# Performance work log

Hardware: AMD Instinct MI355X
Metric: run time of the kernel (lower is better)

## Reference

```python
import jax, jax.numpy as jnp
import numpy as np

B, S, D, H = 128, 256, 256, 8   # graphs, nodes/graph, dim_h, heads
N = B * S
E = 524288
DH = D // H
BN_EPS = 1e-5

def _bn(v, g, b):
    # BatchNorm1d forward with batch statistics (biased var), eval-dropout model
    m = v.mean(0)
    var = v.var(0)
    return (v - m) * jax.lax.rsqrt(var + BN_EPS) * g + b

def setup_inputs() -> dict:
    key = jax.random.key(0)
    ks = jax.random.split(key, 40)
    x = jax.random.normal(ks[0], (N, D), jnp.float32)
    src = jax.random.randint(ks[1], (E,), 0, N)
    dst = (src // S) * S + jax.random.randint(ks[2], (E,), 0, S)  # intra-graph edges
    edge_index = jnp.stack([src, dst]).astype(jnp.int64)
    def lin(k, i, o):
        return (jax.random.normal(k, (i, o), jnp.float32) / np.float32(np.sqrt(i)))
    inp = {
        'x': x, 'edge_index': edge_index,
        'W_gcn': lin(ks[3], D, D), 'b_gcn': jnp.zeros((D,), jnp.float32),
        'W_gin1': lin(ks[4], D, D), 'b_gin1': jnp.zeros((D,), jnp.float32),
        'W_gin2': lin(ks[5], D, D), 'b_gin2': jnp.zeros((D,), jnp.float32),
        'g_kv': jnp.ones((D,), jnp.float32), 'be_kv': jnp.zeros((D,), jnp.float32),
        'Wq1': lin(ks[6], D, D), 'bq1': jnp.zeros((D,), jnp.float32),
        'Wq2': lin(ks[7], D, D), 'bq2': jnp.zeros((D,), jnp.float32),
        'Wq_a': lin(ks[8], D, D), 'bq_a': jnp.zeros((D,), jnp.float32),
        'Wk_a': lin(ks[9], D, D), 'bk_a': jnp.zeros((D,), jnp.float32),
        'Wv_a': lin(ks[10], D, D), 'bv_a': jnp.zeros((D,), jnp.float32),
        'Wo_a': lin(ks[11], D, D), 'bo_a': jnp.zeros((D,), jnp.float32),
        'g_attn': jnp.ones((D,), jnp.float32), 'be_attn': jnp.zeros((D,), jnp.float32),
        'Wf1': lin(ks[12], D, 2 * D), 'bf1': jnp.zeros((2 * D,), jnp.float32),
        'Wf2': lin(ks[13], 2 * D, D), 'bf2': jnp.zeros((D,), jnp.float32),
        'g2': jnp.ones((D,), jnp.float32), 'be2': jnp.zeros((D,), jnp.float32),
    }
    return inp

def _forward(x, edge_index,
             W_gcn, b_gcn, W_gin1, b_gin1, W_gin2, b_gin2, g_kv, be_kv,
             Wq1, bq1, Wq2, bq2,
             Wq_a, bq_a, Wk_a, bk_a, Wv_a, bv_a, Wo_a, bo_a, g_attn, be_attn,
             Wf1, bf1, Wf2, bf2, g2, be2):
    row, col = edge_index[0], edge_index[1]
    h_in1 = x

    # ---- expert 0: GCNConv (add self loops + symmetric norm) ----
    loops = jnp.arange(N, dtype=row.dtype)
    row2 = jnp.concatenate([row, loops])
    col2 = jnp.concatenate([col, loops])
    deg = jax.ops.segment_sum(jnp.ones_like(row2, jnp.float32), col2, num_segments=N)
    dinv = jnp.where(deg > 0, jax.lax.rsqrt(deg), 0.0)
    norm = dinv[row2] * dinv[col2]                     # [E+N]
    xw = x @ W_gcn                                      # [N, D]
    h_gcn = jax.ops.segment_sum(norm[:, None] * xw[row2], col2, num_segments=N) + b_gcn
    e0 = _bn(h_gcn, g_kv, be_kv)

    # ---- expert 1: GINConv (eps=0, sum aggregation, 2-layer MLP) ----
    agg = jax.ops.segment_sum(x[row], col, num_segments=N)
    h_gin = jax.nn.relu((x + agg) @ W_gin1 + b_gin1) @ W_gin2 + b_gin2
    e1 = _bn(h_gin, g_kv, be_kv)

    # ---- global expert normalization (torch .std -> unbiased) ----
    allo = jnp.concatenate([e0, e1], axis=0)
    gm = allo.mean()
    gs = jnp.std(allo, ddof=1)
    e0 = (e0 - gm) / (gs + 1e-8)
    e1 = (e1 - gm) / (gs + 1e-8)

    # ---- uniform routing & kv residual mix ----
    kv = 0.5 * e0 + 0.5 * e1 + 0.1 * h_in1              # [N, D]

    # ---- dense batching (equal-sized graphs -> pure reshape, full mask) ----
    q_dense = h_in1.reshape(B, S, D)
    kv_dense = kv.reshape(B, S, D)

    # ---- q projection MLP ----
    q_dense = jax.nn.relu(q_dense @ Wq1 + bq1) @ Wq2 + bq2

    # ---- multihead attention (batch_first, no padding) ----
    qh = (q_dense @ Wq_a + bq_a).reshape(B, S, H, DH)
    kh = (kv_dense @ Wk_a + bk_a).reshape(B, S, H, DH)
    vh = (kv_dense @ Wv_a + bv_a).reshape(B, S, H, DH)
    scores = jnp.einsum('bqhd,bkhd->bhqk', qh, kh) / np.float32(np.sqrt(DH))
    attn = jax.nn.softmax(scores, axis=-1)
    o = jnp.einsum('bhqk,bkhd->bqhd', attn, vh).reshape(B, S, D)
    h_attn = (o @ Wo_a + bo_a).reshape(N, D)

    # ---- residual + norm + FFN block ----
    h = _bn(h_in1 + h_attn, g_attn, be_attn)
    h_ff = jax.nn.relu(h @ Wf1 + bf1) @ Wf2 + bf2
    h = _bn(h + h_ff, g2, be2)
    return h

def reference(x, edge_index,
              W_gcn, b_gcn, W_gin1, b_gin1, W_gin2, b_gin2, g_kv, be_kv,
              Wq1, bq1, Wq2, bq2,
              Wq_a, bq_a, Wk_a, bk_a, Wv_a, bv_a, Wo_a, bo_a, g_attn, be_attn,
              Wf1, bf1, Wf2, bf2, g2, be2):
    return _forward(x, edge_index,
                    W_gcn, b_gcn, W_gin1, b_gin1, W_gin2, b_gin2, g_kv, be_kv,
                    Wq1, bq1, Wq2, bq2,
                    Wq_a, bq_a, Wk_a, bk_a, Wv_a, bv_a, Wo_a, bo_a, g_attn, be_attn,
                    Wf1, bf1, Wf2, bf2, g2, be2)
```

## Files before the change

### kernel.cpp

```cpp
#include <hip/hip_runtime.h>
#include <hip/hip_bf16.h>

typedef __hip_bfloat16 bf16;
typedef __attribute__((ext_vector_type(8))) short short8;
typedef __attribute__((ext_vector_type(4))) short short4v;
typedef __attribute__((ext_vector_type(4))) float f32x4;
typedef __attribute__((ext_vector_type(4))) int i32x4;

#define N_ 32768
#define D_ 256
#define S_ 256
#define B_ 128
#define E_ 524288

static __device__ __forceinline__ f32x4 mfma16(short8 a, short8 b, f32x4 c) {
  return __builtin_amdgcn_mfma_f32_16x16x32_bf16(a, b, c, 0, 0, 0);
}
static __device__ __forceinline__ f32x4 fzero4() {
  f32x4 z; z[0] = 0.f; z[1] = 0.f; z[2] = 0.f; z[3] = 0.f; return z;
}
static __device__ __forceinline__ float bits2f(short s) {
  unsigned u = ((unsigned)(unsigned short)s) << 16;
  return __builtin_bit_cast(float, u);
}
static __device__ __forceinline__ short f2bits(float f) {
  bf16 b = __float2bfloat16(f);
  return __builtin_bit_cast(short, b);
}

#define GLOAD_LDS16(G, L) __builtin_amdgcn_global_load_lds( \
    (const __attribute__((address_space(1))) void*)(G),     \
    (__attribute__((address_space(3))) void*)(L), 16, 0, 0)

template<int F>
__global__ __launch_bounds__(256)
void gemm_bt(const bf16* __restrict__ A, const bf16* __restrict__ Bt,
             const float* __restrict__ bias, const float* __restrict__ biasB,
             const void* __restrict__ resid,
             float* __restrict__ Cf, bf16* __restrict__ Cb,
             float* __restrict__ Sp, float* __restrict__ SSp,
             int M, int Nc, int K, long bsA, long bsB, long bsC)
{
  __shared__ __align__(16) bf16 lA[2 * 128 * 32];
  __shared__ __align__(16) bf16 lB[2 * 128 * 32];
  __shared__ float sS[2][128], sSS[2][128];
  const int z = blockIdx.z;
  const bf16* Ab = A + (long)z * bsA;
  const bf16* Bb = Bt + (long)z * bsB;
  const int m0 = blockIdx.x * 128, n0 = blockIdx.y * 128;
  const int tid = threadIdx.x;
  const int lane = tid & 63;
  const int w = tid >> 6, wr = w >> 1, wc = w & 1;
  const int g = lane >> 4, r = lane & 15, ko = g * 8;
  const int srow = lane >> 2, skw = (lane & 3) * 8;

  f32x4 acc[4][4];
  for (int i = 0; i < 4; i++) for (int j = 0; j < 4; j++) acc[i][j] = fzero4();

  for (int i = 0; i < 2; i++) {
    const int c = w * 2 + i;
    GLOAD_LDS16(Ab + (long)(m0 + c * 16 + srow) * K + skw, lA + c * 512);
    GLOAD_LDS16(Bb + (long)(n0 + c * 16 + srow) * K + skw, lB + c * 512);
  }
  __syncthreads();

  for (int k0 = 0; k0 < K; k0 += 32) {
    const int cur = (k0 >> 5) & 1, nxt = cur ^ 1;
    if (k0 + 32 < K) {
      for (int i = 0; i < 2; i++) {
        const int c = w * 2 + i;
        GLOAD_LDS16(Ab + (long)(m0 + c * 16 + srow) * K + (k0 + 32) + skw,
                    lA + nxt * 4096 + c * 512);
        GLOAD_LDS16(Bb + (long)(n0 + c * 16 + srow) * K + (k0 + 32) + skw,
                    lB + nxt * 4096 + c * 512);
      }
    }
    short8 af[4], bfv[4];
    for (int mi = 0; mi < 4; mi++)
      af[mi] = *(const short8*)&lA[cur * 4096 + (wr * 64 + mi * 16 + r) * 32 + ko];
    for (int ni = 0; ni < 4; ni++)
      bfv[ni] = *(const short8*)&lB[cur * 4096 + (wc * 64 + ni * 16 + r) * 32 + ko];
    for (int mi = 0; mi < 4; mi++)
      for (int ni = 0; ni < 4; ni++)
        acc[mi][ni] = mfma16(af[mi], bfv[ni], acc[mi][ni]);
    __syncthreads();
  }

  float cs[4] = {0, 0, 0, 0}, css[4] = {0, 0, 0, 0};
  for (int mi = 0; mi < 4; mi++) for (int ni = 0; ni < 4; ni++) {
    const int row = m0 + wr * 64 + mi * 16 + g * 4;
    const int col = n0 + wc * 64 + ni * 16 + r;
    float bv = 0.0f;
    if (F & 2) {
      if ((F & 128) && col >= 256) bv = biasB[col - 256];
      else bv = bias[col];
    }
    for (int j = 0; j < 4; j++) {
      long idx = (long)(row + j) * Nc + col;
      float v = acc[mi][ni][j] + bv;
      if (F & 4)  v += ((const float*)resid)[(long)z * bsC + idx];
      if (F & 64) v += bits2f(((const short*)resid)[(long)z * bsC + idx]);
      if (F & 1)  v = fmaxf(v, 0.0f);
      if (F & 32) { cs[ni] += v; css[ni] += v * v; }
      if (F & 8)  Cf[(long)z * bsC + idx] = v;
      if (F & 16) Cb[(long)z * bsC + idx] = __float2bfloat16(v);
    }
  }
  if (F & 32) {
    for (int ni = 0; ni < 4; ni++) {
      cs[ni]  += __shfl_xor(cs[ni], 16);  cs[ni]  += __shfl_xor(cs[ni], 32);
      css[ni] += __shfl_xor(css[ni], 16); css[ni] += __shfl_xor(css[ni], 32);
    }
    if (lane < 16) {
      for (int ni = 0; ni < 4; ni++) {
        sS[wr][wc * 64 + ni * 16 + lane]  = cs[ni];
        sSS[wr][wc * 64 + ni * 16 + lane] = css[ni];
      }
    }
    __syncthreads();
    if (tid < 128) {
      atomicAdd(&Sp[n0 + tid],  sS[0][tid] + sS[1][tid]);
      atomicAdd(&SSp[n0 + tid], sSS[0][tid] + sSS[1][tid]);
    }
  }
}

template<int NS, int EP1, int EP2, bool STATS>
static __device__ __forceinline__ void mlp_body(
    const bf16* __restrict__ A, const bf16* __restrict__ B1,
    const bf16* __restrict__ B2, const bf16* __restrict__ B3,
    const float* __restrict__ bEp1, const float* __restrict__ bEp2,
    const float* __restrict__ bFin, const bf16* __restrict__ resid,
    bf16* __restrict__ out, float* __restrict__ Sp, float* __restrict__ SSp,
    bf16* lA, bf16* lB, bf16* lC)
{
  char* lCc = (char*)lC;
  const int tid = threadIdx.x;
  const int lane = tid & 63;
  const int w = tid >> 6;
  const int mh = w >> 2, nq = w & 3;
  const int g = lane >> 4, r = lane & 15, ko = g * 8;

  f32x4 acc[2][4];
  for (int i = 0; i < 2; i++) for (int j = 0; j < 4; j++) acc[i][j] = fzero4();

  if (tid < 256)
    GLOAD_LDS16(A + (long)(tid >> 2) * 256 + (tid & 3) * 8, lA + w * 512);
  GLOAD_LDS16(B1 + (long)(tid >> 2) * 256 + (tid & 3) * 8, lB + w * 512);
  GLOAD_LDS16(B1 + (long)((tid + 512) >> 2) * 256 + ((tid + 512) & 3) * 8,
              lB + w * 512 + 4096);
  __syncthreads();
  for (int k0 = 0; k0 < 256; k0 += 32) {
    const int cur = (k0 >> 5) & 1, nxt = cur ^ 1;
    if (k0 + 32 < 256) {
      if (tid < 256)
        GLOAD_LDS16(A + (long)(tid >> 2) * 256 + (k0 + 32) + (tid & 3) * 8,
                    lA + nxt * 2048 + w * 512);
      GLOAD_LDS16(B1 + (long)(tid >> 2) * 256 + (k0 + 32) + (tid & 3) * 8,
                  lB + nxt * 8192 + w * 512);
      GLOAD_LDS16(B1 + (long)((tid + 512) >> 2) * 256 + (k0 + 32) + ((tid + 512) & 3) * 8,
                  lB + nxt * 8192 + w * 512 + 4096);
    }
    short8 af[2], bfv[4];
    for (int mi = 0; mi < 2; mi++)
      af[mi] = *(const short8*)&lA[cur * 2048 + (mh * 32 + mi * 16 + r) * 32 + ko];
    for (int ni = 0; ni < 4; ni++)
      bfv[ni] = *(const short8*)&lB[cur * 8192 + (nq * 64 + ni * 16 + r) * 32 + ko];
    for (int mi = 0; mi < 2; mi++)
      for (int ni = 0; ni < 4; ni++)
        acc[mi][ni] = mfma16(af[mi], bfv[ni], acc[mi][ni]);
    __syncthreads();
  }
  for (int mi = 0; mi < 2; mi++) for (int ni = 0; ni < 4; ni++) {
    const int col = nq * 64 + ni * 16 + r;
    const float bv = (EP1 & 1) ? bEp1[col] : 0.0f;
    for (int j = 0; j < 4; j++) {
      const int row = mh * 32 + mi * 16 + g * 4 + j;
      float v = acc[mi][ni][j] + bv;
      if (EP1 & 4) v += bits2f(__builtin_bit_cast(short, resid[(long)row * 256 + col]));
      if (EP1 & 2) v = fmaxf(v, 0.0f);
      *(short*)(lCc + ((row * 512 + col * 2) ^ ((row & 7) << 4))) = f2bits(v);
    }
  }
  __syncthreads();

  for (int s = 2; s <= NS; s++) {
    const bf16* Bs = (s == 2) ? B2 : B3;
    for (int i = 0; i < 2; i++) for (int j = 0; j < 4; j++) acc[i][j] = fzero4();
    GLOAD_LDS16(Bs + (long)(tid >> 2) * 256 + (tid & 3) * 8, lB + w * 512);
    GLOAD_LDS16(Bs + (long)((tid + 512) >> 2) * 256 + ((tid + 512) & 3) * 8,
                lB + w * 512 + 4096);
    __syncthreads();
    for (int k0 = 0; k0 < 256; k0 += 32) {
      const int cur = (k0 >> 5) & 1, nxt = cur ^ 1;
      if (k0 + 32 < 256) {
        GLOAD_LDS16(Bs + (long)(tid >> 2) * 256 + (k0 + 32) + (tid & 3) * 8,
                    lB + nxt * 8192 + w * 512);
        GLOAD_LDS16(Bs + (long)((tid + 512) >> 2) * 256 + (k0 + 32) + ((tid + 512) & 3) * 8,
                    lB + nxt * 8192 + w * 512 + 4096);
      }
      short8 af[2], bfv[4];
      for (int mi = 0; mi < 2; mi++) {
        const int row = mh * 32 + mi * 16 + r;
        af[mi] = *(const short8*)(lCc +
                  ((row * 512 + (k0 + ko) * 2) ^ ((row & 7) << 4)));
      }
      for (int ni = 0; ni < 4; ni++)
        bfv[ni] = *(const short8*)&lB[cur * 8192 + (nq * 64 + ni * 16 + r) * 32 + ko];
      for (int mi = 0; mi < 2; mi++)
        for (int ni = 0; ni < 4; ni++)
          acc[mi][ni] = mfma16(af[mi], bfv[ni], acc[mi][ni]);
      __syncthreads();
    }
    if (s < NS) {
      for (int mi = 0; mi < 2; mi++) for (int ni = 0; ni < 4; ni++) {
        const int col = nq * 64 + ni * 16 + r;
        const float bv = (EP2 & 1) ? bEp2[col] : 0.0f;
        for (int j = 0; j < 4; j++) {
          const int row = mh * 32 + mi * 16 + g * 4 + j;
          float v = acc[mi][ni][j] + bv;
          if (EP2 & 2) v = fmaxf(v, 0.0f);
          *(short*)(lCc + ((row * 512 + col * 2) ^ ((row & 7) << 4))) = f2bits(v);
        }
      }
      __syncthreads();
    }
  }

  float cs[4] = {0, 0, 0, 0}, css[4] = {0, 0, 0, 0};
  for (int mi = 0; mi < 2; mi++) for (int ni = 0; ni < 4; ni++) {
    const int col = nq * 64 + ni * 16 + r;
    const float bv = bFin[col];
    for (int j = 0; j < 4; j++) {
      const int row = mh * 32 + mi * 16 + g * 4 + j;
      float v = acc[mi][ni][j] + bv;
      if (STATS) { cs[ni] += v; css[ni] += v * v; }
      out[(long)row * 256 + col] = __float2bfloat16(v);
    }
  }
  if (STATS) {
    for (int ni = 0; ni < 4; ni++) {
      cs[ni]  += __shfl_xor(cs[ni], 16);  cs[ni]  += __shfl_xor(cs[ni], 32);
      css[ni] += __shfl_xor(css[ni], 16); css[ni] += __shfl_xor(css[ni], 32);
    }
    __syncthreads();
    float* sS = (float*)lC;
    if (lane < 16) {
      for (int ni = 0; ni < 4; ni++) {
        sS[mh * 256 + nq * 64 + ni * 16 + lane] = cs[ni];
        sS[512 + mh * 256 + nq * 64 + ni * 16 + lane] = css[ni];
      }
    }
    __syncthreads();
    if (tid < 256) {
      atomicAdd(&Sp[tid],  sS[tid] + sS[256 + tid]);
      atomicAdd(&SSp[tid], sS[512 + tid] + sS[768 + tid]);
    }
  }
}

__global__ __launch_bounds__(512)
void fused3_k(const bf16* __restrict__ adjGCNb, const bf16* __restrict__ adjGINb,
              const bf16* __restrict__ xT, const bf16* __restrict__ xb,
              const bf16* __restrict__ WgcnT, const bf16* __restrict__ Wgin1T,
              const bf16* __restrict__ Wgin2T, const bf16* __restrict__ Wq1T,
              const bf16* __restrict__ Wq2T, const bf16* __restrict__ WqaT,
              const float* __restrict__ b_gcn, const float* __restrict__ b_gin1,
              const float* __restrict__ b_gin2, const float* __restrict__ bq1,
              const float* __restrict__ bq2, const float* __restrict__ bq_a,
              bf16* __restrict__ hgcnb, bf16* __restrict__ hginb,
              bf16* __restrict__ qhb,
              float* __restrict__ S0, float* __restrict__ SS0,
              float* __restrict__ S1, float* __restrict__ SS1)
{
  __shared__ __align__(16) bf16 lA[2 * 64 * 32];
  __shared__ __align__(16) bf16 lB[2 * 256 * 32];
  __shared__ __align__(16) bf16 lC[64 * 256];
  const int bid = blockIdx.x;
  if (bid < 512) {
    const long g = bid >> 2;
    mlp_body<2, 0, 0, true>(adjGCNb + (long)bid * 16384, xT + g * 65536,
        WgcnT, nullptr, nullptr, nullptr, b_gcn, nullptr,
        hgcnb + (long)bid * 16384, S0, SS0, lA, lB, lC);
  } else if (bid < 1024) {
    const int sub = bid - 512;
    const long g = sub >> 2;
    mlp_body<3, 4, 3, true>(adjGINb + (long)sub * 16384, xT + g * 65536,
        Wgin1T, Wgin2T, nullptr, b_gin1, b_gin2, xb + (long)sub * 16384,
        hginb + (long)sub * 16384, S1, SS1, lA, lB, lC);
  } else {
    const int sub = bid - 1024;
    mlp_body<3, 3, 1, false>(xb + (long)sub * 16384, Wq1T, Wq2T, WqaT,
        bq1, bq2, bq_a, nullptr, qhb + (long)sub * 16384, nullptr, nullptr,
        lA, lB, lC);
  }
}

__global__ __launch_bounds__(256, 2)
void attn_k(const bf16* __restrict__ qh, const bf16* __restrict__ kh,
            const bf16* __restrict__ vh, bf16* __restrict__ ob, int ks)
{
  const int h = blockIdx.x, qhf = blockIdx.y, b = blockIdx.z;
  const int tid = threadIdx.x, lane = tid & 63, w = tid >> 6;
  const int g = lane >> 4, r = lane & 15, ko = g * 8;
  __shared__ __align__(16) bf16 lK[256 * 32];
  __shared__ __align__(16) bf16 lV[32 * 256];
  char* lKc = (char*)lK;
  char* lVc = (char*)lV;

  for (int i = 0; i < 4; i++) {
    int c = tid + i * 256;
    int row = c >> 2, p4 = c & 3;
    short8 v = *(const short8*)(kh + (long)(b * 256 + row) * ks + h * 32 + p4 * 8);
    *(short8*)(lKc + ((row * 64 + p4 * 16) ^ ((row & 7) << 4))) = v;
  }
  for (int i = 0; i < 2; i++) {
    int c = tid + i * 256;
    int sp = c >> 2, part = c & 3;
    const bf16* vp = vh + (long)(b * 256 + 2 * sp) * ks + h * 32 + part * 8;
    short8 va = *(const short8*)(vp);
    short8 vb = *(const short8*)(vp + ks);
    #pragma unroll
    for (int j = 0; j < 8; j++) {
      int dh = part * 8 + j;
      int sw = ((dh & 7) ^ ((dh >> 3) << 1)) & 7;
      unsigned wrd = ((unsigned)(unsigned short)vb[j] << 16) |
                     (unsigned)(unsigned short)va[j];
      *(unsigned*)(lVc + ((dh * 512 + sp * 4) ^ (sw << 4))) = wrd;
    }
  }
  __syncthreads();

  const float c1 = 0.17677669529663687f * 1.4426950408889634f;
  const int idx0 = (((lane >> 4) & 1) * 32 + r) * 4;
  const int idx1 = idx0 + 64;
  const bool selhi = lane >= 32;

  for (int mc = 0; mc < 2; mc++) {
    const long qbase = (long)b * 256 + qhf * 128 + w * 32 + mc * 16;
    short8 qf = *(const short8*)(qh + (qbase + r) * 256 + h * 32 + ko);
    f32x4 sc[16];
    __builtin_amdgcn_s_setprio(1);
    #pragma unroll
    for (int nc = 0; nc < 16; nc++) {
      int row = nc * 16 + r;
      short8 kf = *(const short8*)(lKc + ((row * 64 + g * 16) ^ ((r & 7) << 4)));
      sc[nc] = mfma16(kf, qf, fzero4());
    }
    __builtin_amdgcn_s_setprio(0);
    f32x4 m4 = sc[0];
    #pragma unroll
    for (int nc = 1; nc < 16; nc++)
      for (int j = 0; j < 4; j++) m4[j] = fmaxf(m4[j], sc[nc][j]);
    float mx = fmaxf(fmaxf(m4[0], m4[1]), fmaxf(m4[2], m4[3]));
    mx = fmaxf(mx, __shfl_xor(mx, 16));
    mx = fmaxf(mx, __shfl_xor(mx, 32));
    const float mxc = mx * c1;
    f32x4 s4 = fzero4();
    #pragma unroll
    for (int nc = 0; nc < 16; nc++)
      for (int j = 0; j < 4; j++) {
        float p = exp2f(fmaf(sc[nc][j], c1, -mxc));
        sc[nc][j] = p; s4[j] += p;
      }
    float sum = s4[0] + s4[1] + s4[2] + s4[3];
    sum += __shfl_xor(sum, 16);
    sum += __shfl_xor(sum, 32);
    const float invs = 1.0f / sum;
    f32x4 oa[2]; oa[0] = fzero4(); oa[1] = fzero4();
    __builtin_amdgcn_s_setprio(1);
    #pragma unroll
    for (int kc = 0; kc < 8; kc++) {
      int pkA0, pkA1, pkB0, pkB1;
      {
        const f32x4 pa = sc[2 * kc], pb = sc[2 * kc + 1];
        unsigned a0 = (unsigned short)f2bits(pa[0] * invs);
        unsigned a1 = (unsigned short)f2bits(pa[1] * invs);
        unsigned a2 = (unsigned short)f2bits(pa[2] * invs);
        unsigned a3 = (unsigned short)f2bits(pa[3] * invs);
        unsigned b0 = (unsigned short)f2bits(pb[0] * invs);
        unsigned b1 = (unsigned short)f2bits(pb[1] * invs);
        unsigned b2 = (unsigned short)f2bits(pb[2] * invs);
        unsigned b3 = (unsigned short)f2bits(pb[3] * invs);
        pkA0 = (int)((a1 << 16) | a0);
        pkA1 = (int)((a3 << 16) | a2);
        pkB0 = (int)((b1 << 16) | b0);
        pkB1 = (int)((b3 << 16) | b2);
      }
      int A0 = __builtin_amdgcn_ds_bpermute(idx0, pkA0);
      int A1 = __builtin_amdgcn_ds_bpermute(idx0, pkA1);
      int B0 = __builtin_amdgcn_ds_bpermute(idx0, pkB0);
      int B1 = __builtin_amdgcn_ds_bpermute(idx0, pkB1);
      int C0 = __builtin_amdgcn_ds_bpermute(idx1, pkA0);
      int C1 = __builtin_amdgcn_ds_bpermute(idx1, pkA1);
      int D0 = __builtin_amdgcn_ds_bpermute(idx1, pkB0);
      int D1 = __builtin_amdgcn_ds_bpermute(idx1, pkB1);
      i32x4 av;
      av[0] = selhi ? B0 : A0;
      av[1] = selhi ? B1 : A1;
      av[2] = selhi ? D0 : C0;
      av[3] = selhi ? D1 : C1;
      short8 af = __builtin_bit_cast(short8, av);
      #pragma unroll
      for (int n = 0; n < 2; n++) {
        int dh = n * 16 + r;
        int sw = ((dh & 7) ^ ((dh >> 3) << 1)) & 7;
        short8 bv = *(const short8*)(lVc + ((dh * 512 + kc * 64 + g * 16) ^ (sw << 4)));
        oa[n] = mfma16(af, bv, oa[n]);
      }
    }
    __builtin_amdgcn_s_setprio(0);
    #pragma unroll
    for (int n = 0; n < 2; n++)
      for (int j = 0; j < 4; j++)
        ob[(qbase + g * 4 + j) * 256 + h * 32 + n * 16 + r] =
          __float2bfloat16(oa[n][j]);
  }
}

__global__ __launch_bounds__(256)
void wprep_k(const float* w0, const float* w1, const float* w2, const float* w3,
             const float* w4, const float* w5, const float* w6, const float* w7,
             const float* w8, const float* wf1, const float* wf2,
             bf16* __restrict__ wT)
{
  __shared__ float tile[32][33];
  const float* srcs[9] = {w0, w1, w2, w3, w4, w5, w6, w7, w8};
  const int bid = blockIdx.x;
  const float* in; bf16* out; int in_rs, out_rs, bx, by;
  if (bid < 576) {
    int wi = bid >> 6, t = bid & 63;
    in = srcs[wi]; out = wT + (long)wi * 65536;
    in_rs = 256; out_rs = 256; bx = t & 7; by = t >> 3;
  } else if (bid < 704) {
    int t = bid - 576;
    in = wf1; out = wT + 589824;
    in_rs = 512; out_rs = 256; bx = t & 15; by = t >> 4;
  } else {
    int t = bid - 704;
    in = wf2; out = wT + 720896;
    in_rs = 256; out_rs = 512; bx = t & 7; by = t >> 3;
  }
  const int tx = threadIdx.x, ty = threadIdx.y;
  const int c = bx * 32 + tx;
  const int rb = by * 32;
  for (int i = 0; i < 4; i++)
    tile[ty + i * 8][tx] = in[(long)(rb + ty + i * 8) * in_rs + c];
  __syncthreads();
  const int oc = rb + tx;
  const int orb = bx * 32;
  for (int i = 0; i < 4; i++)
    out[(long)(orb + ty + i * 8) * out_rs + oc] =
      __float2bfloat16(tile[tx][ty + i * 8]);
}

__global__ __launch_bounds__(256)
void xprep_k(const float* __restrict__ x, bf16* __restrict__ xb,
             bf16* __restrict__ xT)
{
  __shared__ float tile[32][33];
  const int z = blockIdx.z;
  const long ioff = (long)z * 65536;
  const int tx = threadIdx.x, ty = threadIdx.y;
  const int c = blockIdx.x * 32 + tx;
  const int rb = blockIdx.y * 32;
  for (int i = 0; i < 4; i++) {
    float v = x[ioff + (long)(rb + ty + i * 8) * 256 + c];
    tile[ty + i * 8][tx] = v;
    xb[ioff + (long)(rb + ty + i * 8) * 256 + c] = __float2bfloat16(v);
  }
  __syncthreads();
  const int oc = rb + tx;
  const int orb = blockIdx.x * 32;
  for (int i = 0; i < 4; i++)
    xT[ioff + (long)(orb + ty + i * 8) * 256 + oc] =
      __float2bfloat16(tile[tx][ty + i * 8]);
}

__global__ __launch_bounds__(256)
void edge_cnt_k(const int* __restrict__ ei, unsigned* __restrict__ cnt)
{
  int e = blockIdx.x * 256 + threadIdx.x;
  int src = ei[e], dst = ei[E_ + e];
  long idx = ((long)(src >> 8) * 256 + (dst & 255)) * 256 + (src & 255);
  atomicAdd(&cnt[idx >> 2], 1u << ((idx & 3) * 8));
}

__global__ __launch_bounds__(256)
void deg_k(const unsigned* __restrict__ cnt, float* __restrict__ dinv)
{
  int rid = blockIdx.x * 16 + (threadIdx.x >> 4);
  int l16 = threadIdx.x & 15;
  uint4 v = ((const uint4*)(cnt + (long)rid * 64))[l16];
  unsigned s = 0;
  s += (v.x & 0xFF) + ((v.x >> 8) & 0xFF) + ((v.x >> 16) & 0xFF) + (v.x >> 24);
  s += (v.y & 0xFF) + ((v.y >> 8) & 0xFF) + ((v.y >> 16) & 0xFF) + (v.y >> 24);
  s += (v.z & 0xFF) + ((v.z >> 8) & 0xFF) + ((v.z >> 16) & 0xFF) + (v.z >> 24);
  s += (v.w & 0xFF) + ((v.w >> 8) & 0xFF) + ((v.w >> 16) & 0xFF) + (v.w >> 24);
  s += __shfl_xor(s, 1); s += __shfl_xor(s, 2);
  s += __shfl_xor(s, 4); s += __shfl_xor(s, 8);
  if (l16 == 0) dinv[rid] = rsqrtf((float)s + 1.0f);
}

__global__ __launch_bounds__(256)
void adj_derive_k(const unsigned* __restrict__ cnt, const float* __restrict__ dinv,
                  bf16* __restrict__ gin, bf16* __restrict__ gcn)
{
  long wi = (long)blockIdx.x * 256 + threadIdx.x;
  unsigned cw = cnt[wi];
  long i = wi * 4;
  float cv[4] = {(float)(cw & 0xFF), (float)((cw >> 8) & 0xFF),
                 (float)((cw >> 16) & 0xFF), (float)(cw >> 24)};
  long row = i >> 8;
  int g = (int)(row >> 8), dst = (int)(row & 255);
  int src0 = (int)(i & 255);
  float dd = dinv[row];
  const float* ds = dinv + (long)g * 256 + src0;
  short4v oi, oc;
  for (int j = 0; j < 4; j++) {
    float gv = cv[j] * dd * ds[j];
    if (src0 + j == dst) gv += dd * dd;
    oi[j] = f2bits(cv[j]);
    oc[j] = f2bits(gv);
  }
  *(short4v*)(gin + i) = oi;
  *(short4v*)(gcn + i) = oc;
}

__global__ __launch_bounds__(256)
void expert_stats_k(const float* __restrict__ S0, const float* __restrict__ SS0,
                    const float* __restrict__ S1, const float* __restrict__ SS1,
                    const float* __restrict__ gkv, const float* __restrict__ bkv,
                    float* __restrict__ kA, float* __restrict__ kB,
                    float* __restrict__ kC)
{
  const int d = threadIdx.x;
  const float invN = 1.0f / 32768.0f;
  float m0 = S0[d] * invN, v0 = SS0[d] * invN - m0 * m0;
  float a0 = gkv[d] * rsqrtf(v0 + 1e-5f), c0 = bkv[d] - m0 * a0;
  float m1 = S1[d] * invN, v1 = SS1[d] * invN - m1 * m1;
  float a1 = gkv[d] * rsqrtf(v1 + 1e-5f), c1 = bkv[d] - m1 * a1;
  float gsum = a0 * S0[d] + 32768.0f * c0 + a1 * S1[d] + 32768.0f * c1;
  float gss  = a0 * a0 * SS0[d] + 2.0f * a0 * c0 * S0[d] + 32768.0f * c0 * c0
             + a1 * a1 * SS1[d] + 2.0f * a1 * c1 * S1[d] + 32768.0f * c1 * c1;
  __shared__ float r1[256], r2[256];
  r1[d] = gsum; r2[d] = gss;
  __syncthreads();
  for (int s = 128; s > 0; s >>= 1) {
    if (d < s) { r1[d] += r1[d + s]; r2[d] += r2[d + s]; }
    __syncthreads();
  }
  const float cntall = 16777216.0f;
  float tg = r1[0], tss = r2[0];
  float gm = tg / cntall;
  float var = (tss - tg * tg / cntall) / (cntall - 1.0f);
  float gs = sqrtf(fmaxf(var, 0.f)) + 1e-8f;
  kA[d] = 0.5f * a0 / gs;
  kB[d] = 0.5f * a1 / gs;
  kC[d] = 0.5f * (c0 + c1 - 2.0f * gm) / gs;
}

__global__ __launch_bounds__(256)
void kv_mix_k(const bf16* __restrict__ hgcn, const bf16* __restrict__ hgin,
              const bf16* __restrict__ xb, const float* __restrict__ kA,
              const float* __restrict__ kB, const float* __restrict__ kC,
              bf16* __restrict__ kv)
{
  long i = ((long)blockIdx.x * 256 + threadIdx.x) * 8;
  int d0 = (int)(i & 255);
  short8 a = *(const short8*)(hgcn + i);
  short8 b = *(const short8*)(hgin + i);
  short8 c = *(const short8*)(xb + i);
  short8 o;
  for (int j = 0; j < 8; j++) {
    int d = d0 + j;
    float v = kA[d] * bits2f(a[j]) + kB[d] * bits2f(b[j]) + kC[d] + 0.1f * bits2f(c[j]);
    o[j] = f2bits(v);
  }
  *(short8*)(kv + i) = o;
}

template<int MODE>
__global__ __launch_bounds__(256)
void bn_apply_k(const bf16* __restrict__ in, const float* __restrict__ S,
                const float* __restrict__ SSq, const float* __restrict__ gg,
                const float* __restrict__ bb, float* __restrict__ outf,
                bf16* __restrict__ outb)
{
  long i = ((long)blockIdx.x * 256 + threadIdx.x) * 8;
  int d0 = (int)(i & 255);
  short8 v = *(const short8*)(in + i);
  const float invN = 1.0f / 32768.0f;
  float4 o0, o1; short8 o8;
  for (int j = 0; j < 8; j++) {
    int d = d0 + j;
    float m = S[d] * invN;
    float var = SSq[d] * invN - m * m;
    float a = gg[d] * rsqrtf(var + 1e-5f);
    float c = bb[d] - m * a;
    float o = a * bits2f(v[j]) + c;
    if (MODE & 1) { if (j < 4) (&o0.x)[j] = o; else (&o1.x)[j - 4] = o; }
    if (MODE & 2) o8[j] = f2bits(o);
  }
  if (MODE & 1) { *(float4*)(outf + i) = o0; *(float4*)(outf + i + 4) = o1; }
  if (MODE & 2) *(short8*)(outb + i) = o8;
}

static constexpr size_t OFF_S0 = 0, OFF_SS0 = 1024, OFF_S1 = 2048, OFF_SS1 = 3072;
static constexpr size_t OFF_S2 = 4096, OFF_SS2 = 5120, OFF_S3 = 6144, OFF_SS3 = 7168;
static constexpr size_t OFF_KA = 8192, OFF_KB = 9216, OFF_KC = 10240;
static constexpr size_t OFF_CNT = 16384;
static constexpr size_t CNT_BYTES = (size_t)B_ * S_ * S_;
static constexpr size_t ZERO_BYTES = OFF_CNT + CNT_BYTES;
static constexpr size_t OFF_DINV = OFF_CNT + (size_t)B_ * S_ * S_ * 2;
static constexpr size_t OFF_W = OFF_DINV + 131072;
static constexpr size_t NDB2 = (size_t)N_ * D_ * 2;
static constexpr size_t OFF_ADJGINB = OFF_W + 1703936;
static constexpr size_t OFF_ADJGCNB = OFF_ADJGINB + NDB2;
static constexpr size_t OFF_XB   = OFF_ADJGCNB + NDB2;
static constexpr size_t OFF_XT   = OFF_XB + NDB2;
static constexpr size_t OFF_AGG  = OFF_XT + NDB2;
static constexpr size_t OFF_GIN  = OFF_AGG + NDB2;
static constexpr size_t OFF_KV   = OFF_GIN + NDB2;
static constexpr size_t OFF_HGCN = OFF_KV + NDB2;
static constexpr size_t OFF_HGIN = OFF_HGCN + NDB2;

extern "C" void kernel_launch(void* const* d_in, const int* in_sizes, int n_in,
                              void* d_out, int out_size, void* d_ws, size_t ws_size,
                              hipStream_t stream)
{
  (void)in_sizes; (void)n_in; (void)out_size; (void)ws_size;
  const float* x      = (const float*)d_in[0];
  const int*   ei     = (const int*)d_in[1];
  const float* W_gcn  = (const float*)d_in[2];
  const float* b_gcn  = (const float*)d_in[3];
  const float* W_gin1 = (const float*)d_in[4];
  const float* b_gin1 = (const float*)d_in[5];
  const float* W_gin2 = (const float*)d_in[6];
  const float* b_gin2 = (const float*)d_in[7];
  const float* g_kv   = (const float*)d_in[8];
  const float* be_kv  = (const float*)d_in[9];
  const float* Wq1    = (const float*)d_in[10];
  const float* bq1    = (const float*)d_in[11];
  const float* Wq2    = (const float*)d_in[12];
  const float* bq2    = (const float*)d_in[13];
  const float* Wq_a   = (const float*)d_in[14];
  const float* bq_a   = (const float*)d_in[15];
  const float* Wk_a   = (const float*)d_in[16];
  const float* bk_a   = (const float*)d_in[17];
  const float* Wv_a   = (const float*)d_in[18];
  const float* bv_a   = (const float*)d_in[19];
  const float* Wo_a   = (const float*)d_in[20];
  const float* bo_a   = (const float*)d_in[21];
  const float* g_attn = (const float*)d_in[22];
  const float* be_attn= (const float*)d_in[23];
  const float* Wf1    = (const float*)d_in[24];
  const float* bf1    = (const float*)d_in[25];
  const float* Wf2    = (const float*)d_in[26];
  const float* bf2    = (const float*)d_in[27];
  const float* g2     = (const float*)d_in[28];
  const float* be2    = (const float*)d_in[29];

  char* ws = (char*)d_ws;
  float* S0  = (float*)(ws + OFF_S0);  float* SS0 = (float*)(ws + OFF_SS0);
  float* S1  = (float*)(ws + OFF_S1);  float* SS1 = (float*)(ws + OFF_SS1);
  float* S2  = (float*)(ws + OFF_S2);  float* SS2 = (float*)(ws + OFF_SS2);
  float* S3  = (float*)(ws + OFF_S3);  float* SS3 = (float*)(ws + OFF_SS3);
  float* kA  = (float*)(ws + OFF_KA);  float* kB  = (float*)(ws + OFF_KB);
  float* kC  = (float*)(ws + OFF_KC);
  unsigned* cntA = (unsigned*)(ws + OFF_CNT);
  float* dinv = (float*)(ws + OFF_DINV);
  bf16* wT = (bf16*)(ws + OFF_W);
  bf16 *WgcnT = wT,            *Wgin1T = wT + 65536,  *Wgin2T = wT + 131072;
  bf16 *Wq1T  = wT + 196608,   *Wq2T   = wT + 262144, *WqaT   = wT + 327680;
  bf16 *WkaT  = wT + 393216,   *WoaT   = wT + 524288;
  bf16 *Wf1T  = wT + 589824,   *Wf2T   = wT + 720896;
  bf16* adjGINb = (bf16*)(ws + OFF_ADJGINB);
  bf16* adjGCNb = (bf16*)(ws + OFF_ADJGCNB);
  bf16* xb    = (bf16*)(ws + OFF_XB);
  bf16* xT    = (bf16*)(ws + OFF_XT);
  bf16* kv_bf = (bf16*)(ws + OFF_KV);
  bf16* hgcnb = (bf16*)(ws + OFF_HGCN);
  bf16* hginb = (bf16*)(ws + OFF_HGIN);
  bf16* qhb    = (bf16*)(ws + OFF_CNT);
  bf16* khvb   = (bf16*)(ws + OFF_AGG);
  bf16* ob     = hginb;
  bf16* tbufb  = (bf16*)(ws + OFF_CNT);
  bf16* hb     = xb;
  bf16* f1b    = adjGINb;
  bf16* t2b    = (bf16*)(ws + OFF_CNT);
  float* outp  = (float*)d_out;

  hipMemsetAsync(d_ws, 0, ZERO_BYTES, stream);

  dim3 tb(32, 8);
  wprep_k<<<832, tb, 0, stream>>>(W_gcn, W_gin1, W_gin2, Wq1, Wq2,
                                  Wq_a, Wk_a, Wv_a, Wo_a, Wf1, Wf2, wT);
  xprep_k<<<dim3(8, 8, 128), tb, 0, stream>>>(x, xb, xT);
  edge_cnt_k<<<2048, 256, 0, stream>>>(ei, cntA);
  deg_k<<<2048, 256, 0, stream>>>(cntA, dinv);
  adj_derive_k<<<8192, 256, 0, stream>>>(cntA, dinv, adjGINb, adjGCNb);
  fused3_k<<<1536, 512, 0, stream>>>(adjGCNb, adjGINb, xT, xb,
      WgcnT, Wgin1T, Wgin2T, Wq1T, Wq2T, WqaT,
      b_gcn, b_gin1, b_gin2, bq1, bq2, bq_a,
      hgcnb, hginb, qhb, S0, SS0, S1, SS1);
  expert_stats_k<<<1, 256, 0, stream>>>(S0, SS0, S1, SS1, g_kv, be_kv, kA, kB, kC);
  kv_mix_k<<<4096, 256, 0, stream>>>(hgcnb, hginb, xb, kA, kB, kC, kv_bf);
  gemm_bt<146><<<dim3(256, 4, 1), 256, 0, stream>>>(kv_bf, WkaT, bk_a, bv_a,
      nullptr, nullptr, khvb, nullptr, nullptr, N_, 512, 256, 0, 0, 0);
  attn_k<<<dim3(8, 2, 128), 256, 0, stream>>>(qhb, khvb, khvb + 256, ob, 512);
  gemm_bt<114><<<dim3(256, 2, 1), 256, 0, stream>>>(ob, WoaT, bo_a, nullptr,
      xb, nullptr, tbufb, S2, SS2, N_, 256, 256, 0, 0, 0);
  bn_apply_k<2><<<4096, 256, 0, stream>>>(tbufb, S2, SS2, g_attn, be_attn, nullptr, hb);
  gemm_bt<19><<<dim3(256, 4, 1), 256, 0, stream>>>(hb, Wf1T, bf1, nullptr,
      nullptr, nullptr, f1b, nullptr, nullptr, N_, 512, 256, 0, 0, 0);
  gemm_bt<114><<<dim3(256, 2, 1), 256, 0, stream>>>(f1b, Wf2T, bf2, nullptr,
      hb, nullptr, t2b, S3, SS3, N_, 256, 512, 0, 0, 0);
  bn_apply_k<1><<<4096, 256, 0, stream>>>(t2b, S3, SS3, g2, be2, outp, nullptr);
}
```

Measured before the change: 308.9 us.

## Merge prep kernels, fuse degree into adjacency build, raise MFMA priority, simplify V staging

Folds the weight transpose, x conversion and edge counting into one launch, and fuses the degree computation and adjacency derivation into a per-graph kernel that keeps inverse degrees in shared memory. This cuts launch count and removes a global round trip for dinv. It also wraps the MFMA loops in s_setprio so matrix work is favoured over other waves, and changes attention V staging to 16-bit LDS stores with one global load per row. The per-graph kernel runs only 128 blocks, which may leave the GPU underused, and the 16-bit LDS stores double the number of store instructions.

```diff
diff --git a/kernel.cpp b/kernel.cpp
--- a/kernel.cpp
+++ b/kernel.cpp
@@ -80,9 +80,11 @@
       af[mi] = *(const short8*)&lA[cur * 4096 + (wr * 64 + mi * 16 + r) * 32 + ko];
     for (int ni = 0; ni < 4; ni++)
       bfv[ni] = *(const short8*)&lB[cur * 4096 + (wc * 64 + ni * 16 + r) * 32 + ko];
+    __builtin_amdgcn_s_setprio(1);
     for (int mi = 0; mi < 4; mi++)
       for (int ni = 0; ni < 4; ni++)
         acc[mi][ni] = mfma16(af[mi], bfv[ni], acc[mi][ni]);
+    __builtin_amdgcn_s_setprio(0);
     __syncthreads();
   }
 
@@ -166,9 +168,11 @@
       af[mi] = *(const short8*)&lA[cur * 2048 + (mh * 32 + mi * 16 + r) * 32 + ko];
     for (int ni = 0; ni < 4; ni++)
       bfv[ni] = *(const short8*)&lB[cur * 8192 + (nq * 64 + ni * 16 + r) * 32 + ko];
+    __builtin_amdgcn_s_setprio(1);
     for (int mi = 0; mi < 2; mi++)
       for (int ni = 0; ni < 4; ni++)
         acc[mi][ni] = mfma16(af[mi], bfv[ni], acc[mi][ni]);
+    __builtin_amdgcn_s_setprio(0);
     __syncthreads();
   }
   for (int mi = 0; mi < 2; mi++) for (int ni = 0; ni < 4; ni++) {
@@ -207,9 +211,11 @@
       }
       for (int ni = 0; ni < 4; ni++)
         bfv[ni] = *(const short8*)&lB[cur * 8192 + (nq * 64 + ni * 16 + r) * 32 + ko];
+      __builtin_amdgcn_s_setprio(1);
       for (int mi = 0; mi < 2; mi++)
         for (int ni = 0; ni < 4; ni++)
           acc[mi][ni] = mfma16(af[mi], bfv[ni], acc[mi][ni]);
+      __builtin_amdgcn_s_setprio(0);
       __syncthreads();
     }
     if (s < NS) {
@@ -314,19 +320,15 @@
     short8 v = *(const short8*)(kh + (long)(b * 256 + row) * ks + h * 32 + p4 * 8);
     *(short8*)(lKc + ((row * 64 + p4 * 16) ^ ((row & 7) << 4))) = v;
   }
-  for (int i = 0; i < 2; i++) {
+  for (int i = 0; i < 4; i++) {
     int c = tid + i * 256;
-    int sp = c >> 2, part = c & 3;
-    const bf16* vp = vh + (long)(b * 256 + 2 * sp) * ks + h * 32 + part * 8;
-    short8 va = *(const short8*)(vp);
-    short8 vb = *(const short8*)(vp + ks);
+    int s = c >> 2, part = c & 3;
+    short8 v = *(const short8*)(vh + (long)(b * 256 + s) * ks + h * 32 + part * 8);
     #pragma unroll
     for (int j = 0; j < 8; j++) {
       int dh = part * 8 + j;
       int sw = ((dh & 7) ^ ((dh >> 3) << 1)) & 7;
-      unsigned wrd = ((unsigned)(unsigned short)vb[j] << 16) |
-                     (unsigned)(unsigned short)va[j];
-      *(unsigned*)(lVc + ((dh * 512 + sp * 4) ^ (sw << 4))) = wrd;
+      *(short*)(lVc + ((dh * 512 + s * 2) ^ (sw << 4))) = v[j];
     }
   }
   __syncthreads();
@@ -419,112 +421,110 @@
 }
 
 __global__ __launch_bounds__(256)
-void wprep_k(const float* w0, const float* w1, const float* w2, const float* w3,
-             const float* w4, const float* w5, const float* w6, const float* w7,
-             const float* w8, const float* wf1, const float* wf2,
-             bf16* __restrict__ wT)
+void prep_k(const float* w0, const float* w1, const float* w2, const float* w3,
+            const float* w4, const float* w5, const float* w6, const float* w7,
+            const float* w8, const float* wf1, const float* wf2,
+            bf16* __restrict__ wT,
+            const float* __restrict__ x, bf16* __restrict__ xb,
+            bf16* __restrict__ xT,
+            const int* __restrict__ ei, unsigned* __restrict__ cnt)
 {
   __shared__ float tile[32][33];
-  const float* srcs[9] = {w0, w1, w2, w3, w4, w5, w6, w7, w8};
   const int bid = blockIdx.x;
-  const float* in; bf16* out; int in_rs, out_rs, bx, by;
-  if (bid < 576) {
-    int wi = bid >> 6, t = bid & 63;
-    in = srcs[wi]; out = wT + (long)wi * 65536;
-    in_rs = 256; out_rs = 256; bx = t & 7; by = t >> 3;
-  } else if (bid < 704) {
-    int t = bid - 576;
-    in = wf1; out = wT + 589824;
-    in_rs = 512; out_rs = 256; bx = t & 15; by = t >> 4;
+  const int tid = threadIdx.x;
+  const int tx = tid & 31, ty = tid >> 5;
+
+  if (bid < 832) {
+    const float* srcs[9] = {w0, w1, w2, w3, w4, w5, w6, w7, w8};
+    const float* in; bf16* out; int in_rs, out_rs, bx, by;
+    if (bid < 576) {
+      int wi = bid >> 6, t = bid & 63;
+      in = srcs[wi]; out = wT + (long)wi * 65536;
+      in_rs = 256; out_rs = 256; bx = t & 7; by = t >> 3;
+    } else if (bid < 704) {
+      int t = bid - 576;
+      in = wf1; out = wT + 589824;
+      in_rs = 512; out_rs = 256; bx = t & 15; by = t >> 4;
+    } else {
+      int t = bid - 704;
+      in = wf2; out = wT + 720896;
+      in_rs = 256; out_rs = 512; bx = t & 7; by = t >> 3;
+    }
+    const int c = bx * 32 + tx;
+    const int rb = by * 32;
+    for (int i = 0; i < 4; i++)
+      tile[ty + i * 8][tx] = in[(long)(rb + ty + i * 8) * in_rs + c];
+    __syncthreads();
+    const int oc = rb + tx;
+    const int orb = bx * 32;
+    for (int i = 0; i < 4; i++)
+      out[(long)(orb + ty + i * 8) * out_rs + oc] =
+        __float2bfloat16(tile[tx][ty + i * 8]);
+  } else if (bid < 9024) {
+    const int b2 = bid - 832;
+    const int z = b2 >> 6, bx = b2 & 7, by = (b2 >> 3) & 7;
+    const long ioff = (long)z * 65536;
+    const int c = bx * 32 + tx;
+    const int rb = by * 32;
+    for (int i = 0; i < 4; i++) {
+      float v = x[ioff + (long)(rb + ty + i * 8) * 256 + c];
+      tile[ty + i * 8][tx] = v;
+      xb[ioff + (long)(rb + ty + i * 8) * 256 + c] = __float2bfloat16(v);
+    }
+    __syncthreads();
+    const int oc = rb + tx;
+    const int orb = bx * 32;
+    for (int i = 0; i < 4; i++)
+      xT[ioff + (long)(orb + ty + i * 8) * 256 + oc] =
+        __float2bfloat16(tile[tx][ty + i * 8]);
   } else {
-    int t = bid - 704;
-    in = wf2; out = wT + 720896;
-    in_rs = 256; out_rs = 512; bx = t & 7; by = t >> 3;
-  }
-  const int tx = threadIdx.x, ty = threadIdx.y;
-  const int c = bx * 32 + tx;
-  const int rb = by * 32;
-  for (int i = 0; i < 4; i++)
-    tile[ty + i * 8][tx] = in[(long)(rb + ty + i * 8) * in_rs + c];
+    int e = (bid - 9024) * 256 + tid;
+    int src = ei[e], dst = ei[E_ + e];
+    long idx = ((long)(src >> 8) * 256 + (dst & 255)) * 256 + (src & 255);
+    atomicAdd(&cnt[idx >> 2], 1u << ((idx & 3) * 8));
+  }
+}
+
+__global__ __launch_bounds__(256)
+void graph_prep_k(const unsigned* __restrict__ cnt,
+                  bf16* __restrict__ gin, bf16* __restrict__ gcn)
+{
+  __shared__ float sdinv[256];
+  const int gg = blockIdx.x, tid = threadIdx.x;
+  const unsigned* cg = cnt + (long)gg * 16384;
+  const int l16 = tid & 15, rg = tid >> 4;
+  for (int p = 0; p < 16; p++) {
+    const int row = p * 16 + rg;
+    uint4 v = ((const uint4*)(cg + (long)row * 64))[l16];
+    unsigned s = 0;
+    s += (v.x & 0xFF) + ((v.x >> 8) & 0xFF) + ((v.x >> 16) & 0xFF) + (v.x >> 24);
+    s += (v.y & 0xFF) + ((v.y >> 8) & 0xFF) + ((v.y >> 16) & 0xFF) + (v.y >> 24);
+    s += (v.z & 0xFF) + ((v.z >> 8) & 0xFF) + ((v.z >> 16) & 0xFF) + (v.z >> 24);
+    s += (v.w & 0xFF) + ((v.w >> 8) & 0xFF) + ((v.w >> 16) & 0xFF) + (v.w >> 24);
+    s += __shfl_xor(s, 1); s += __shfl_xor(s, 2);
+    s += __shfl_xor(s, 4); s += __shfl_xor(s, 8);
+    if (l16 == 0) sdinv[row] = rsqrtf((float)s + 1.0f);
+  }
   __syncthreads();
-  const int oc = rb + tx;
-  const int orb = bx * 32;
-  for (int i = 0; i < 4; i++)
-    out[(long)(orb + ty + i * 8) * out_rs + oc] =
-      __float2bfloat16(tile[tx][ty + i * 8]);
-}
-
-__global__ __launch_bounds__(256)
-void xprep_k(const float* __restrict__ x, bf16* __restrict__ xb,
-             bf16* __restrict__ xT)
-{
-  __shared__ float tile[32][33];
-  const int z = blockIdx.z;
-  const long ioff = (long)z * 65536;
-  const int tx = threadIdx.x, ty = threadIdx.y;
-  const int c = blockIdx.x * 32 + tx;
-  const int rb = blockIdx.y * 32;
-  for (int i = 0; i < 4; i++) {
-    float v = x[ioff + (long)(rb + ty + i * 8) * 256 + c];
-    tile[ty + i * 8][tx] = v;
-    xb[ioff + (long)(rb + ty + i * 8) * 256 + c] = __float2bfloat16(v);
-  }
-  __syncthreads();
-  const int oc = rb + tx;
-  const int orb = blockIdx.x * 32;
-  for (int i = 0; i < 4; i++)
-    xT[ioff + (long)(orb + ty + i * 8) * 256 + oc] =
-      __float2bfloat16(tile[tx][ty + i * 8]);
-}
-
-__global__ __launch_bounds__(256)
-void edge_cnt_k(const int* __restrict__ ei, unsigned* __restrict__ cnt)
-{
-  int e = blockIdx.x * 256 + threadIdx.x;
-  int src = ei[e], dst = ei[E_ + e];
-  long idx = ((long)(src >> 8) * 256 + (dst & 255)) * 256 + (src & 255);
-  atomicAdd(&cnt[idx >> 2], 1u << ((idx & 3) * 8));
-}
-
-__global__ __launch_bounds__(256)
-void deg_k(const unsigned* __restrict__ cnt, float* __restrict__ dinv)
-{
-  int rid = blockIdx.x * 16 + (threadIdx.x >> 4);
-  int l16 = threadIdx.x & 15;
-  uint4 v = ((const uint4*)(cnt + (long)rid * 64))[l16];
-  unsigned s = 0;
-  s += (v.x & 0xFF) + ((v.x >> 8) & 0xFF) + ((v.x >> 16) & 0xFF) + (v.x >> 24);
-  s += (v.y & 0xFF) + ((v.y >> 8) & 0xFF) + ((v.y >> 16) & 0xFF) + (v.y >> 24);
-  s += (v.z & 0xFF) + ((v.z >> 8) & 0xFF) + ((v.z >> 16) & 0xFF) + (v.z >> 24);
-  s += (v.w & 0xFF) + ((v.w >> 8) & 0xFF) + ((v.w >> 16) & 0xFF) + (v.w >> 24);
-  s += __shfl_xor(s, 1); s += __shfl_xor(s, 2);
-  s += __shfl_xor(s, 4); s += __shfl_xor(s, 8);
-  if (l16 == 0) dinv[rid] = rsqrtf((float)s + 1.0f);
-}
-
-__global__ __launch_bounds__(256)
-void adj_derive_k(const unsigned* __restrict__ cnt, const float* __restrict__ dinv,
-                  bf16* __restrict__ gin, bf16* __restrict__ gcn)
-{
-  long wi = (long)blockIdx.x * 256 + threadIdx.x;
-  unsigned cw = cnt[wi];
-  long i = wi * 4;
-  float cv[4] = {(float)(cw & 0xFF), (float)((cw >> 8) & 0xFF),
-                 (float)((cw >> 16) & 0xFF), (float)(cw >> 24)};
-  long row = i >> 8;
-  int g = (int)(row >> 8), dst = (int)(row & 255);
-  int src0 = (int)(i & 255);
-  float dd = dinv[row];
-  const float* ds = dinv + (long)g * 256 + src0;
-  short4v oi, oc;
-  for (int j = 0; j < 4; j++) {
-    float gv = cv[j] * dd * ds[j];
-    if (src0 + j == dst) gv += dd * dd;
-    oi[j] = f2bits(cv[j]);
-    oc[j] = f2bits(gv);
-  }
-  *(short4v*)(gin + i) = oi;
-  *(short4v*)(gcn + i) = oc;
+  for (int p = 0; p < 64; p++) {
+    const int wl = p * 256 + tid;
+    const unsigned cw = cg[wl];
+    const long i = ((long)gg * 16384 + wl) * 4;
+    const int cell = wl * 4;
+    const int dst = cell >> 8, src0 = cell & 255;
+    const float dd = sdinv[dst];
+    float cv[4] = {(float)(cw & 0xFF), (float)((cw >> 8) & 0xFF),
+                   (float)((cw >> 16) & 0xFF), (float)(cw >> 24)};
+    short4v oi, oc;
+    for (int j = 0; j < 4; j++) {
+      float gv = cv[j] * dd * sdinv[src0 + j];
+      if (src0 + j == dst) gv += dd * dd;
+      oi[j] = f2bits(cv[j]);
+      oc[j] = f2bits(gv);
+    }
+    *(short4v*)(gin + i) = oi;
+    *(short4v*)(gcn + i) = oc;
+  }
 }
 
 __global__ __launch_bounds__(256)
@@ -669,7 +669,6 @@
   float* kA  = (float*)(ws + OFF_KA);  float* kB  = (float*)(ws + OFF_KB);
   float* kC  = (float*)(ws + OFF_KC);
   unsigned* cntA = (unsigned*)(ws + OFF_CNT);
-  float* dinv = (float*)(ws + OFF_DINV);
   bf16* wT = (bf16*)(ws + OFF_W);
   bf16 *WgcnT = wT,            *Wgin1T = wT + 65536,  *Wgin2T = wT + 131072;
   bf16 *Wq1T  = wT + 196608,   *Wq2T   = wT + 262144, *WqaT   = wT + 327680;
@@ -693,13 +692,9 @@
 
   hipMemsetAsync(d_ws, 0, ZERO_BYTES, stream);
 
-  dim3 tb(32, 8);
-  wprep_k<<<832, tb, 0, stream>>>(W_gcn, W_gin1, W_gin2, Wq1, Wq2,
-                                  Wq_a, Wk_a, Wv_a, Wo_a, Wf1, Wf2, wT);
-  xprep_k<<<dim3(8, 8, 128), tb, 0, stream>>>(x, xb, xT);
-  edge_cnt_k<<<2048, 256, 0, stream>>>(ei, cntA);
-  deg_k<<<2048, 256, 0, stream>>>(cntA, dinv);
-  adj_derive_k<<<8192, 256, 0, stream>>>(cntA, dinv, adjGINb, adjGCNb);
+  prep_k<<<11072, 256, 0, stream>>>(W_gcn, W_gin1, W_gin2, Wq1, Wq2,
+      Wq_a, Wk_a, Wv_a, Wo_a, Wf1, Wf2, wT, x, xb, xT, ei, cntA);
+  graph_prep_k<<<128, 256, 0, stream>>>(cntA, adjGINb, adjGCNb);
   fused3_k<<<1536, 512, 0, stream>>>(adjGCNb, adjGINb, xT, xb,
       WgcnT, Wgin1T, Wgin2T, Wq1T, Wq2T, WqaT,
       b_gcn, b_gin1, b_gin2, bq1, bq2, bq_a,
```

After: 314.8 us. Within noise of the previous version (+1.9%).
